# Kernel optimization log

Measured on AMD Instinct MI355X. Metric: run time of the kernel, lower is better.

The kernel has to match this reference:

```python
import jax, jax.numpy as jnp
import numpy as np

N = 500_000
E = 8_000_000
F = 16


def setup_inputs() -> dict:
    key = jax.random.key(0)
    ks = jax.random.split(key, 8)
    x = jax.random.normal(ks[0], (N, F), dtype=jnp.float32)
    h0 = jax.random.normal(ks[1], (N, F), dtype=jnp.float32)
    adj_row = jnp.sort(jax.random.randint(ks[2], (E,), 0, N, dtype=jnp.int32)).astype(jnp.int64)
    adj_col = jax.random.randint(ks[3], (E,), 0, N, dtype=jnp.int32).astype(jnp.int64)
    adj_val = jax.random.uniform(ks[4], (E,), dtype=jnp.float32)
    stdv = 1.0 / np.sqrt(F)
    weight = jax.random.uniform(ks[5], (2 * F, F), minval=-stdv, maxval=stdv, dtype=jnp.float32)
    fc_w = jax.random.normal(ks[6], (1, F), dtype=jnp.float32) * 0.1
    fc_b = jax.random.normal(ks[7], (1,), dtype=jnp.float32) * 0.1
    lamda = jnp.ones((1,), dtype=jnp.float32) * 0.5
    l = 2
    return {"x": x, "h0": h0, "adj_row": adj_row, "adj_col": adj_col,
            "adj_val": adj_val, "weight": weight, "fc_w": fc_w, "fc_b": fc_b,
            "lamda": lamda, "l": l}


def reference(x, h0, adj_row, adj_col, adj_val, weight, fc_w, fc_b, lamda, l):
    n = x.shape[0]
    # sparse aggregation: hi = A @ x  (COO spmm via gather + segment_sum)
    hi = jax.ops.segment_sum(adj_val[:, None] * x[adj_col], adj_row, num_segments=n)  # [N, F]
    # small MLP gate: alpha = Linear(16,1)(hi)
    alpha = hi @ fc_w.T + fc_b  # [N, 1]
    theta = jnp.log(lamda / l + 1.0)  # [1], broadcasts
    support = jnp.concatenate([hi, h0], axis=1)  # [N, 2F] (variant=True)
    r = (1.0 - alpha) * hi + alpha * h0  # [N, F]
    out = theta * (support @ weight) + (1.0 - theta) * r
    return out + x  # residual=True
```

## Files before the change

### kernel.cpp

```cpp
#include <hip/hip_runtime.h>

#define FDIM 16
#define RPB  32
#define NG   32
#define CAP  1024

__global__ __launch_bounds__(256) void rowptr_kernel(const int* __restrict__ rows,
                                                     int* __restrict__ row_ptr,
                                                     long long nedge, int n) {
  long long e = (long long)blockIdx.x * blockDim.x + threadIdx.x;
  if (e >= nedge) return;
  int b = rows[e];
  if (e == 0) {
    for (int r = 0; r <= b; ++r) row_ptr[r] = 0;
  } else {
    int a = rows[e - 1];
    for (int r = a + 1; r <= b; ++r) row_ptr[r] = (int)e;
  }
  if (e == nedge - 1) {
    for (int r = b + 1; r <= n; ++r) row_ptr[r] = (int)nedge;
  }
}

__global__ __launch_bounds__(256) void spmm_fuse_kernel(
    const int* __restrict__ row_ptr,
    const int* __restrict__ rows,
    const int* __restrict__ cols,
    const float* __restrict__ vals,
    const float* __restrict__ x,
    const float* __restrict__ h0,
    const float* __restrict__ weight,
    const float* __restrict__ fc_w,
    const float* __restrict__ fc_b,
    const float* __restrict__ lamda,
    const int* __restrict__ lpar,
    float* __restrict__ out,
    int n) {
  __shared__ float wsh[2 * FDIM * FDIM];
  __shared__ int   lr[CAP];
  __shared__ int   lc[CAP];
  __shared__ float lv[CAP];
  __shared__ float lhi[RPB][FDIM];

  int tid = (int)threadIdx.x;
  for (int i = tid; i < 2 * FDIM * FDIM; i += 256) wsh[i] = weight[i];
  for (int i = tid; i < RPB * FDIM; i += 256) ((float*)lhi)[i] = 0.f;

  int g = tid >> 3;
  int l = tid & 7;
  int R0 = blockIdx.x * RPB;
  int Rend = min(R0 + RPB, n);
  int r = R0 + g;

  int s_blk = row_ptr[R0];
  int t_blk = row_ptr[Rend];

  __syncthreads();

  const float2* __restrict__ x2 = reinterpret_cast<const float2*>(x);

  for (int t0 = s_blk; t0 < t_blk; t0 += CAP) {
    int t1 = min(t0 + CAP, t_blk);
    int len = t1 - t0;
    for (int i = tid; i < len; i += 256) {
      lr[i] = rows[t0 + i] - R0;
      lc[i] = cols[t0 + i];
      lv[i] = vals[t0 + i];
    }
    __syncthreads();

    int a = (len * g) >> 5;
    int b = (len * (g + 1)) >> 5;
    if (a < b) {
      int cur = lr[a];
      float ax = 0.f, ay = 0.f;

#define FLUSH()                                   \
      { atomicAdd(&lhi[cur][2 * l],     ax);      \
        atomicAdd(&lhi[cur][2 * l + 1], ay);      \
        ax = 0.f; ay = 0.f; }
#define STEP(r_, v_, gx_, gy_)                    \
      if (r_ != cur) { FLUSH(); cur = r_; }       \
      ax = fmaf(v_, gx_, ax);                     \
      ay = fmaf(v_, gy_, ay);

      int e = a;
      for (; e + 8 <= b; e += 8) {
        int   r0 = lr[e+0], r1 = lr[e+1], r2 = lr[e+2], r3 = lr[e+3];
        int   r4 = lr[e+4], r5 = lr[e+5], r6 = lr[e+6], r7 = lr[e+7];
        int   c0 = lc[e+0], c1 = lc[e+1], c2 = lc[e+2], c3 = lc[e+3];
        int   c4 = lc[e+4], c5 = lc[e+5], c6 = lc[e+6], c7 = lc[e+7];
        float v0 = lv[e+0], v1 = lv[e+1], v2 = lv[e+2], v3 = lv[e+3];
        float v4 = lv[e+4], v5 = lv[e+5], v6 = lv[e+6], v7 = lv[e+7];
        float2 g0 = x2[c0 * 8 + l], g1 = x2[c1 * 8 + l];
        float2 g2 = x2[c2 * 8 + l], g3 = x2[c3 * 8 + l];
        float2 g4 = x2[c4 * 8 + l], g5 = x2[c5 * 8 + l];
        float2 g6 = x2[c6 * 8 + l], g7 = x2[c7 * 8 + l];
        if (r7 == cur) {
          ax = fmaf(v0, g0.x, ax); ay = fmaf(v0, g0.y, ay);
          ax = fmaf(v1, g1.x, ax); ay = fmaf(v1, g1.y, ay);
          ax = fmaf(v2, g2.x, ax); ay = fmaf(v2, g2.y, ay);
          ax = fmaf(v3, g3.x, ax); ay = fmaf(v3, g3.y, ay);
          ax = fmaf(v4, g4.x, ax); ay = fmaf(v4, g4.y, ay);
          ax = fmaf(v5, g5.x, ax); ay = fmaf(v5, g5.y, ay);
          ax = fmaf(v6, g6.x, ax); ay = fmaf(v6, g6.y, ay);
          ax = fmaf(v7, g7.x, ax); ay = fmaf(v7, g7.y, ay);
        } else {
          STEP(r0, v0, g0.x, g0.y)
          STEP(r1, v1, g1.x, g1.y)
          STEP(r2, v2, g2.x, g2.y)
          STEP(r3, v3, g3.x, g3.y)
          STEP(r4, v4, g4.x, g4.y)
          STEP(r5, v5, g5.x, g5.y)
          STEP(r6, v6, g6.x, g6.y)
          STEP(r7, v7, g7.x, g7.y)
        }
      }
      for (; e < b; ++e) {
        int rr_ = lr[e];
        float2 gg = x2[lc[e] * 8 + l];
        STEP(rr_, lv[e], gg.x, gg.y)
      }
      FLUSH();
#undef STEP
#undef FLUSH
    }
    __syncthreads();
  }

  __syncthreads();

  if (r >= n) return;

  float2 hi2 = make_float2(lhi[g][2 * l], lhi[g][2 * l + 1]);
  float2 h02 = reinterpret_cast<const float2*>(h0)[(size_t)r * 8 + l];
  float2 xf2 = reinterpret_cast<const float2*>(x)[(size_t)r * 8 + l];
  float theta = logf(lamda[0] / (float)lpar[0] + 1.0f);

  float av = hi2.x * fc_w[2 * l] + hi2.y * fc_w[2 * l + 1];
  av += __shfl_xor(av, 1, 8);
  av += __shfl_xor(av, 2, 8);
  av += __shfl_xor(av, 4, 8);
  float alpha = av + fc_b[0];

  const float2* wsh2 = reinterpret_cast<const float2*>(wsh);
  float sx = 0.f, sy = 0.f;
#pragma unroll
  for (int k = 0; k < FDIM; ++k) {
    float hk  = lhi[g][k];
    float h0k = (k & 1) ? __shfl(h02.y, k >> 1, 8)
                        : __shfl(h02.x, k >> 1, 8);
    float2 w1 = wsh2[k * 8 + l];
    float2 w2 = wsh2[(FDIM + k) * 8 + l];
    sx = fmaf(hk, w1.x, sx);  sy = fmaf(hk, w1.y, sy);
    sx = fmaf(h0k, w2.x, sx); sy = fmaf(h0k, w2.y, sy);
  }

  float rx = (1.f - alpha) * hi2.x + alpha * h02.x;
  float ry = (1.f - alpha) * hi2.y + alpha * h02.y;
  float2 o;
  o.x = fmaf(theta, sx, (1.f - theta) * rx) + xf2.x;
  o.y = fmaf(theta, sy, (1.f - theta) * ry) + xf2.y;
  reinterpret_cast<float2*>(out)[(size_t)r * 8 + l] = o;
}

extern "C" void kernel_launch(void* const* d_in, const int* in_sizes, int n_in,
                              void* d_out, int out_size, void* d_ws, size_t ws_size,
                              hipStream_t stream) {
  const float* x        = (const float*)d_in[0];
  const float* h0       = (const float*)d_in[1];
  const int* adj_row    = (const int*)d_in[2];
  const int* adj_col    = (const int*)d_in[3];
  const float* adj_val  = (const float*)d_in[4];
  const float* weight   = (const float*)d_in[5];
  const float* fc_w     = (const float*)d_in[6];
  const float* fc_b     = (const float*)d_in[7];
  const float* lamda    = (const float*)d_in[8];
  const int* lpar       = (const int*)d_in[9];

  int n = in_sizes[0] / FDIM;
  long long nedge = in_sizes[2];
  float* out = (float*)d_out;
  int* row_ptr = (int*)d_ws;

  long long rb = (nedge + 255) / 256;
  rowptr_kernel<<<(int)rb, 256, 0, stream>>>(adj_row, row_ptr, nedge, n);

  int sb = (n + RPB - 1) / RPB;
  spmm_fuse_kernel<<<sb, 256, 0, stream>>>(row_ptr, adj_row, adj_col, adj_val,
                                           x, h0, weight, fc_w, fc_b, lamda,
                                           lpar, out, n);
}
```

Measured before the change: 174.5 us.

## Drop per-edge row index loads; derive row boundaries from shared row_ptr

The fused SpMM kernel no longer streams adj_row for every edge. It caches the block's slice of row_ptr in shared memory, finds each group's starting row with a binary search, and advances row boundaries by comparing edge indices against row_ptr. Blocks are also enlarged to 512 threads, 64 rows and a 2048-edge staging buffer. This removes about a third of the per-edge global traffic, at the cost of a short serial search per group and more shared memory per block, which may lower occupancy.

```diff
diff --git a/kernel.cpp b/kernel.cpp
--- a/kernel.cpp
+++ b/kernel.cpp
@@ -1,9 +1,9 @@
 #include <hip/hip_runtime.h>
 
 #define FDIM 16
-#define RPB  32
-#define NG   32
-#define CAP  1024
+#define RPB  64
+#define NT   512
+#define CAP  2048
 
 __global__ __launch_bounds__(256) void rowptr_kernel(const int* __restrict__ rows,
                                                      int* __restrict__ row_ptr,
@@ -22,9 +22,8 @@
   }
 }
 
-__global__ __launch_bounds__(256) void spmm_fuse_kernel(
+__global__ __launch_bounds__(NT) void spmm_fuse_kernel(
     const int* __restrict__ row_ptr,
-    const int* __restrict__ rows,
     const int* __restrict__ cols,
     const float* __restrict__ vals,
     const float* __restrict__ x,
@@ -37,57 +36,59 @@
     float* __restrict__ out,
     int n) {
   __shared__ float wsh[2 * FDIM * FDIM];
-  __shared__ int   lr[CAP];
+  __shared__ int   lrp[RPB + 1];
   __shared__ int   lc[CAP];
   __shared__ float lv[CAP];
   __shared__ float lhi[RPB][FDIM];
 
   int tid = (int)threadIdx.x;
-  for (int i = tid; i < 2 * FDIM * FDIM; i += 256) wsh[i] = weight[i];
-  for (int i = tid; i < RPB * FDIM; i += 256) ((float*)lhi)[i] = 0.f;
+  int R0 = blockIdx.x * RPB;
+  for (int i = tid; i < 2 * FDIM * FDIM; i += NT) wsh[i] = weight[i];
+  for (int i = tid; i < RPB * FDIM; i += NT) ((float*)lhi)[i] = 0.f;
+  for (int i = tid; i <= RPB; i += NT) lrp[i] = row_ptr[min(R0 + i, n)];
+  __syncthreads();
 
   int g = tid >> 3;
   int l = tid & 7;
-  int R0 = blockIdx.x * RPB;
-  int Rend = min(R0 + RPB, n);
-  int r = R0 + g;
-
-  int s_blk = row_ptr[R0];
-  int t_blk = row_ptr[Rend];
-
-  __syncthreads();
+  int s_blk = lrp[0];
+  int t_blk = lrp[RPB];
 
   const float2* __restrict__ x2 = reinterpret_cast<const float2*>(x);
 
   for (int t0 = s_blk; t0 < t_blk; t0 += CAP) {
     int t1 = min(t0 + CAP, t_blk);
     int len = t1 - t0;
-    for (int i = tid; i < len; i += 256) {
-      lr[i] = rows[t0 + i] - R0;
+    for (int i = tid; i < len; i += NT) {
       lc[i] = cols[t0 + i];
       lv[i] = vals[t0 + i];
     }
     __syncthreads();
 
-    int a = (len * g) >> 5;
-    int b = (len * (g + 1)) >> 5;
+    int a = (len * g) >> 6;
+    int b = (len * (g + 1)) >> 6;
     if (a < b) {
-      int cur = lr[a];
+      int ge0 = t0 + a;
+      int lo = 0, hi = RPB;
+      while (hi - lo > 1) {
+        int mid = (lo + hi) >> 1;
+        if (lrp[mid] <= ge0) lo = mid; else hi = mid;
+      }
+      int cur = lo;
+      int nxt = lrp[cur + 1];
       float ax = 0.f, ay = 0.f;
 
 #define FLUSH()                                   \
       { atomicAdd(&lhi[cur][2 * l],     ax);      \
         atomicAdd(&lhi[cur][2 * l + 1], ay);      \
         ax = 0.f; ay = 0.f; }
-#define STEP(r_, v_, gx_, gy_)                    \
-      if (r_ != cur) { FLUSH(); cur = r_; }       \
-      ax = fmaf(v_, gx_, ax);                     \
-      ay = fmaf(v_, gy_, ay);
+#define ADV(gl_)                                  \
+      if (gl_ >= nxt) {                           \
+        FLUSH();                                  \
+        do { ++cur; nxt = lrp[cur + 1]; } while (gl_ >= nxt); \
+      }
 
       int e = a;
       for (; e + 8 <= b; e += 8) {
-        int   r0 = lr[e+0], r1 = lr[e+1], r2 = lr[e+2], r3 = lr[e+3];
-        int   r4 = lr[e+4], r5 = lr[e+5], r6 = lr[e+6], r7 = lr[e+7];
         int   c0 = lc[e+0], c1 = lc[e+1], c2 = lc[e+2], c3 = lc[e+3];
         int   c4 = lc[e+4], c5 = lc[e+5], c6 = lc[e+6], c7 = lc[e+7];
         float v0 = lv[e+0], v1 = lv[e+1], v2 = lv[e+2], v3 = lv[e+3];
@@ -96,7 +97,7 @@
         float2 g2 = x2[c2 * 8 + l], g3 = x2[c3 * 8 + l];
         float2 g4 = x2[c4 * 8 + l], g5 = x2[c5 * 8 + l];
         float2 g6 = x2[c6 * 8 + l], g7 = x2[c7 * 8 + l];
-        if (r7 == cur) {
+        if (t0 + e + 7 < nxt) {
           ax = fmaf(v0, g0.x, ax); ay = fmaf(v0, g0.y, ay);
           ax = fmaf(v1, g1.x, ax); ay = fmaf(v1, g1.y, ay);
           ax = fmaf(v2, g2.x, ax); ay = fmaf(v2, g2.y, ay);
@@ -106,23 +107,24 @@
           ax = fmaf(v6, g6.x, ax); ay = fmaf(v6, g6.y, ay);
           ax = fmaf(v7, g7.x, ax); ay = fmaf(v7, g7.y, ay);
         } else {
-          STEP(r0, v0, g0.x, g0.y)
-          STEP(r1, v1, g1.x, g1.y)
-          STEP(r2, v2, g2.x, g2.y)
-          STEP(r3, v3, g3.x, g3.y)
-          STEP(r4, v4, g4.x, g4.y)
-          STEP(r5, v5, g5.x, g5.y)
-          STEP(r6, v6, g6.x, g6.y)
-          STEP(r7, v7, g7.x, g7.y)
+          ADV(t0 + e + 0) ax = fmaf(v0, g0.x, ax); ay = fmaf(v0, g0.y, ay);
+          ADV(t0 + e + 1) ax = fmaf(v1, g1.x, ax); ay = fmaf(v1, g1.y, ay);
+          ADV(t0 + e + 2) ax = fmaf(v2, g2.x, ax); ay = fmaf(v2, g2.y, ay);
+          ADV(t0 + e + 3) ax = fmaf(v3, g3.x, ax); ay = fmaf(v3, g3.y, ay);
+          ADV(t0 + e + 4) ax = fmaf(v4, g4.x, ax); ay = fmaf(v4, g4.y, ay);
+          ADV(t0 + e + 5) ax = fmaf(v5, g5.x, ax); ay = fmaf(v5, g5.y, ay);
+          ADV(t0 + e + 6) ax = fmaf(v6, g6.x, ax); ay = fmaf(v6, g6.y, ay);
+          ADV(t0 + e + 7) ax = fmaf(v7, g7.x, ax); ay = fmaf(v7, g7.y, ay);
         }
       }
       for (; e < b; ++e) {
-        int rr_ = lr[e];
         float2 gg = x2[lc[e] * 8 + l];
-        STEP(rr_, lv[e], gg.x, gg.y)
+        float  vv = lv[e];
+        ADV(t0 + e)
+        ax = fmaf(vv, gg.x, ax); ay = fmaf(vv, gg.y, ay);
       }
       FLUSH();
-#undef STEP
+#undef ADV
 #undef FLUSH
     }
     __syncthreads();
@@ -130,6 +132,7 @@
 
   __syncthreads();
 
+  int r = R0 + g;
   if (r >= n) return;
 
   float2 hi2 = make_float2(lhi[g][2 * l], lhi[g][2 * l + 1]);
@@ -187,7 +190,7 @@
   rowptr_kernel<<<(int)rb, 256, 0, stream>>>(adj_row, row_ptr, nedge, n);
 
   int sb = (n + RPB - 1) / RPB;
-  spmm_fuse_kernel<<<sb, 256, 0, stream>>>(row_ptr, adj_row, adj_col, adj_val,
-                                           x, h0, weight, fc_w, fc_b, lamda,
-                                           lpar, out, n);
+  spmm_fuse_kernel<<<sb, NT, 0, stream>>>(row_ptr, adj_col, adj_val,
+                                          x, h0, weight, fc_w, fc_b, lamda,
+                                          lpar, out, n);
 }
```

Result: no change. 175.1 us (+0.4%).

## Replace row_ptr kernel with per-block wave-wide binary search of sorted rows

Applied to the files above, without the earlier changes.

Removes the separate kernel that builds a CSR row pointer array over all edges. Instead, the first wavefront of each SpMM block finds its edge range with a 64-way ballot-based search over the sorted row indices. This drops one launch and a full pass over the 8M-entry row array, at the cost of a few dependent global-memory search rounds at the start of each block. It also widens the gather index arithmetic to size_t.

```diff
diff --git a/kernel.cpp b/kernel.cpp
--- a/kernel.cpp
+++ b/kernel.cpp
@@ -2,28 +2,27 @@
 
 #define FDIM 16
 #define RPB  32
-#define NG   32
+#define NT   256
 #define CAP  1024
 
-__global__ __launch_bounds__(256) void rowptr_kernel(const int* __restrict__ rows,
-                                                     int* __restrict__ row_ptr,
-                                                     long long nedge, int n) {
-  long long e = (long long)blockIdx.x * blockDim.x + threadIdx.x;
-  if (e >= nedge) return;
-  int b = rows[e];
-  if (e == 0) {
-    for (int r = 0; r <= b; ++r) row_ptr[r] = 0;
-  } else {
-    int a = rows[e - 1];
-    for (int r = a + 1; r <= b; ++r) row_ptr[r] = (int)e;
+__device__ __forceinline__ int lower_bound_wave(const int* __restrict__ rows,
+                                                int nedge, int target, int lane) {
+  int lo = 0, hi = nedge;
+  while (hi > lo) {
+    int step = (hi - lo + 63) >> 6;
+    int idx = lo + lane * step;
+    bool pred = (idx < hi) && (rows[idx] < target);
+    unsigned long long m = __ballot(pred);
+    if (m == 0ULL) { hi = lo; break; }
+    int j = 63 - __builtin_clzll(m);
+    int nlo = lo + j * step + 1;
+    int nhi = (j < 63) ? min(lo + (j + 1) * step, hi) : hi;
+    lo = nlo; hi = nhi;
   }
-  if (e == nedge - 1) {
-    for (int r = b + 1; r <= n; ++r) row_ptr[r] = (int)nedge;
-  }
+  return lo;
 }
 
-__global__ __launch_bounds__(256) void spmm_fuse_kernel(
-    const int* __restrict__ row_ptr,
+__global__ __launch_bounds__(NT) void spmm_fuse_kernel(
     const int* __restrict__ rows,
     const int* __restrict__ cols,
     const float* __restrict__ vals,
@@ -35,34 +34,38 @@
     const float* __restrict__ lamda,
     const int* __restrict__ lpar,
     float* __restrict__ out,
-    int n) {
+    int n, int nedge) {
   __shared__ float wsh[2 * FDIM * FDIM];
   __shared__ int   lr[CAP];
   __shared__ int   lc[CAP];
   __shared__ float lv[CAP];
   __shared__ float lhi[RPB][FDIM];
+  __shared__ int   sbounds[2];
 
   int tid = (int)threadIdx.x;
-  for (int i = tid; i < 2 * FDIM * FDIM; i += 256) wsh[i] = weight[i];
-  for (int i = tid; i < RPB * FDIM; i += 256) ((float*)lhi)[i] = 0.f;
+  int R0 = blockIdx.x * RPB;
+  int Rend = min(R0 + RPB, n);
+
+  if (tid < 64) {
+    int sb = lower_bound_wave(rows, nedge, R0, tid);
+    int tb = lower_bound_wave(rows, nedge, Rend, tid);
+    if (tid == 0) { sbounds[0] = sb; sbounds[1] = tb; }
+  }
+  for (int i = tid; i < 2 * FDIM * FDIM; i += NT) wsh[i] = weight[i];
+  for (int i = tid; i < RPB * FDIM; i += NT) ((float*)lhi)[i] = 0.f;
+  __syncthreads();
+
+  int s_blk = sbounds[0];
+  int t_blk = sbounds[1];
 
   int g = tid >> 3;
   int l = tid & 7;
-  int R0 = blockIdx.x * RPB;
-  int Rend = min(R0 + RPB, n);
-  int r = R0 + g;
-
-  int s_blk = row_ptr[R0];
-  int t_blk = row_ptr[Rend];
-
-  __syncthreads();
-
   const float2* __restrict__ x2 = reinterpret_cast<const float2*>(x);
 
   for (int t0 = s_blk; t0 < t_blk; t0 += CAP) {
     int t1 = min(t0 + CAP, t_blk);
     int len = t1 - t0;
-    for (int i = tid; i < len; i += 256) {
+    for (int i = tid; i < len; i += NT) {
       lr[i] = rows[t0 + i] - R0;
       lc[i] = cols[t0 + i];
       lv[i] = vals[t0 + i];
@@ -92,10 +95,10 @@
         int   c4 = lc[e+4], c5 = lc[e+5], c6 = lc[e+6], c7 = lc[e+7];
         float v0 = lv[e+0], v1 = lv[e+1], v2 = lv[e+2], v3 = lv[e+3];
         float v4 = lv[e+4], v5 = lv[e+5], v6 = lv[e+6], v7 = lv[e+7];
-        float2 g0 = x2[c0 * 8 + l], g1 = x2[c1 * 8 + l];
-        float2 g2 = x2[c2 * 8 + l], g3 = x2[c3 * 8 + l];
-        float2 g4 = x2[c4 * 8 + l], g5 = x2[c5 * 8 + l];
-        float2 g6 = x2[c6 * 8 + l], g7 = x2[c7 * 8 + l];
+        float2 g0 = x2[(size_t)c0 * 8 + l], g1 = x2[(size_t)c1 * 8 + l];
+        float2 g2 = x2[(size_t)c2 * 8 + l], g3 = x2[(size_t)c3 * 8 + l];
+        float2 g4 = x2[(size_t)c4 * 8 + l], g5 = x2[(size_t)c5 * 8 + l];
+        float2 g6 = x2[(size_t)c6 * 8 + l], g7 = x2[(size_t)c7 * 8 + l];
         if (r7 == cur) {
           ax = fmaf(v0, g0.x, ax); ay = fmaf(v0, g0.y, ay);
           ax = fmaf(v1, g1.x, ax); ay = fmaf(v1, g1.y, ay);
@@ -118,7 +121,7 @@
       }
       for (; e < b; ++e) {
         int rr_ = lr[e];
-        float2 gg = x2[lc[e] * 8 + l];
+        float2 gg = x2[(size_t)lc[e] * 8 + l];
         STEP(rr_, lv[e], gg.x, gg.y)
       }
       FLUSH();
@@ -130,6 +133,7 @@
 
   __syncthreads();
 
+  int r = R0 + g;
   if (r >= n) return;
 
   float2 hi2 = make_float2(lhi[g][2 * l], lhi[g][2 * l + 1]);
@@ -179,15 +183,11 @@
   const int* lpar       = (const int*)d_in[9];
 
   int n = in_sizes[0] / FDIM;
-  long long nedge = in_sizes[2];
+  int nedge = in_sizes[2];
   float* out = (float*)d_out;
-  int* row_ptr = (int*)d_ws;
-
-  long long rb = (nedge + 255) / 256;
-  rowptr_kernel<<<(int)rb, 256, 0, stream>>>(adj_row, row_ptr, nedge, n);
 
   int sb = (n + RPB - 1) / RPB;
-  spmm_fuse_kernel<<<sb, 256, 0, stream>>>(row_ptr, adj_row, adj_col, adj_val,
-                                           x, h0, weight, fc_w, fc_b, lamda,
-                                           lpar, out, n);
+  spmm_fuse_kernel<<<sb, NT, 0, stream>>>(adj_row, adj_col, adj_val, x, h0,
+                                          weight, fc_w, fc_b, lamda, lpar,
+                                          out, n, nedge);
 }
```

Measured after the change: 183.3 us. 1.05x slower.
